# Kernel tuning notes

Hardware: AMD Instinct MI355X
Metric: run time of the kernel (lower is better)

## Reference

```python
import jax, jax.numpy as jnp
import numpy as np

DIM = 96        # N_VOX/2^(n_scales-layer) = 384/4 at finest layer
C = 24          # ch_in[2]
N_CUR = 150_000
N_GLB = 300_000
N_TGT = 100_000
N_GTGT = 200_000


def setup_inputs() -> dict:
    key = jax.random.key(0)
    ks = jax.random.split(key, 10)
    current_coords = jax.random.randint(ks[0], (N_CUR, 3), 0, DIM, dtype=jnp.int32)
    current_values = jax.random.normal(ks[1], (N_CUR, C), dtype=jnp.float32)
    # global coords live in the global frame; after subtracting the origin some fall outside [0, DIM)
    global_coords = jax.random.randint(ks[2], (N_GLB, 3), 0, DIM + 14, dtype=jnp.int32)
    global_value = jax.random.normal(ks[3], (N_GLB, C), dtype=jnp.float32)
    coords_target_global = jax.random.randint(ks[4], (N_TGT, 3), 0, DIM, dtype=jnp.int32)
    tsdf_target = jax.random.uniform(ks[5], (N_TGT,), minval=-1.0, maxval=1.0, dtype=jnp.float32)
    global_coords_target = jax.random.randint(ks[6], (N_GTGT, 3), 0, DIM + 14, dtype=jnp.int32)
    global_tsdf_target = jax.random.uniform(ks[7], (N_GTGT, 1), minval=-1.0, maxval=1.0, dtype=jnp.float32)
    relative_origin = jnp.array([5, 5, 5], dtype=jnp.int32)
    grid_mask = jax.random.randint(ks[8], (N_CUR,), 0, 2) > 0
    occupancy = jax.random.randint(ks[9], (N_CUR,), 0, 2) > 0
    return dict(current_coords=current_coords, current_values=current_values,
                global_coords=global_coords, global_value=global_value,
                coords_target_global=coords_target_global, tsdf_target=tsdf_target,
                global_coords_target=global_coords_target, global_tsdf_target=global_tsdf_target,
                relative_origin=relative_origin, grid_mask=grid_mask, occupancy=occupancy)


def _masked_idx(coords, mask, dim):
    # rows with mask==False get an out-of-range index -> dropped by scatter mode='drop'
    return jnp.where(mask[:, None], coords, dim)


def reference(current_coords, current_values, global_coords, global_value,
              coords_target_global, tsdf_target, global_coords_target,
              global_tsdf_target, relative_origin, grid_mask, occupancy):
    dim = DIM
    dtype = current_values.dtype
    c = current_values.shape[-1]

    # ---- shift global coords into local fragment frame; in-bounds test ----
    gc = global_coords - relative_origin                       # (Ng, 3)
    in_bounds = jnp.logical_and(gc >= 0, gc < dim).all(-1)     # (Ng,)

    # ---- valid_volume: True where a current voxel inside the camera frusta exists ----
    vi = _masked_idx(current_coords, grid_mask, dim)
    valid_volume = jnp.zeros((dim, dim, dim), dtype=bool).at[vi[:, 0], vi[:, 1], vi[:, 2]].set(True, mode='drop')

    # gather visibility at (clamped) global coords; out-of-bounds rows masked off
    gcc = jnp.clip(gc, 0, dim - 1)
    valid = in_bounds & valid_volume[gcc[:, 0], gcc[:, 1], gcc[:, 2]]   # == local_visible

    # ---- sparse -> dense feature volumes (feat_init = 0) ----
    gi = _masked_idx(gc, valid, dim)
    global_volume = jnp.zeros((dim, dim, dim, c), dtype=dtype).at[gi[:, 0], gi[:, 1], gi[:, 2]].set(global_value, mode='drop')
    cc = current_coords
    current_volume = jnp.zeros((dim, dim, dim, c), dtype=dtype).at[cc[:, 0], cc[:, 1], cc[:, 2]].set(current_values, mode='drop')

    # ---- occupancy volume & updated coordinate mask (dense mask == nonzero set) ----
    oi = _masked_idx(current_coords, occupancy, dim)
    occ_volume = jnp.zeros((dim, dim, dim), dtype=bool).at[oi[:, 0], oi[:, 1], oi[:, 2]].set(True, mode='drop')
    updated_mask = (global_volume != 0).any(-1) | occ_volume

    # voxels in FBV but not visible in current fragment (near set)
    near_mask = in_bounds & jnp.logical_not(valid)

    # ---- ground-truth TSDF fusion (default value = 1) ----
    gct = global_coords_target - relative_origin
    valid_target = jnp.logical_and(gct >= 0, gct < dim).all(-1)
    ti = _masked_idx(gct, valid_target, dim)
    target_volume = jnp.full((dim, dim, dim, 1), 1.0, dtype=dtype)
    target_volume = target_volume.at[ti[:, 0], ti[:, 1], ti[:, 2]].set(global_tsdf_target, mode='drop')
    ct = coords_target_global
    target_volume = target_volume.at[ct[:, 0], ct[:, 1], ct[:, 2]].set(tsdf_target[:, None], mode='drop')

    return (updated_mask, current_volume, global_volume, target_volume, valid, valid_target, near_mask)
```

## Files before the change

kernel.cpp:

```cpp
#include <hip/hip_runtime.h>

#define DIMV 96
#define CCH 24
#define NVOX (DIMV * DIMV * DIMV)
#define HALFV (NVOX / 2)
#define WORDS (NVOX / 32)
#define ZERO_INTS (2 * WORDS)
#define TOTAL_INTS (ZERO_INTS + 3 * NVOX)
#define N4I (TOTAL_INTS / 4)
#define NZERO4 (ZERO_INTS / 4)

#define PAYLOAD_BLOCKS (HALFV * 6 / 256)
#define MT_BLOCKS (NVOX / 1024)
#define RESOLVE_BLOCKS (PAYLOAD_BLOCKS + MT_BLOCKS)

typedef float v4f __attribute__((ext_vector_type(4)));
typedef int   v4i __attribute__((ext_vector_type(4)));
typedef int   v2i __attribute__((ext_vector_type(2)));

__global__ void init_detect_kernel(v4i* __restrict__ ws_vec,
                                   const unsigned int* __restrict__ mask_words,
                                   int* __restrict__ mode_p) {
    int i = blockIdx.x * blockDim.x + threadIdx.x;
    if (i < N4I) {
        int fill = (i < NZERO4) ? 0 : -1;
        v4i val = {fill, fill, fill, fill};
        ws_vec[i] = val;
    }
    if (blockIdx.x == 0) {
        __shared__ int s_byte, s_int, s_float;
        if (threadIdx.x == 0) { s_byte = 0; s_int = 0; s_float = 0; }
        __syncthreads();
        int flag = 0;
        for (int k = 0; k < 4; ++k) {
            unsigned int w = mask_words[threadIdx.x * 4 + k];
            if (w != 0u) {
                if (w == 1u)               flag |= 1;
                else if (w == 0x3F800000u) flag |= 2;
                else                       flag |= 4;
            }
        }
        if (flag & 1) atomicOr(&s_int, 1);
        if (flag & 2) atomicOr(&s_float, 1);
        if (flag & 4) atomicOr(&s_byte, 1);
        __syncthreads();
        if (threadIdx.x == 0)
            *mode_p = s_byte ? 0 : (s_float ? 2 : 1);
    }
}

__device__ __forceinline__ bool read_mask(const void* p, int i, int mode) {
    if (mode == 0) return ((const unsigned char*)p)[i] != 0;
    if (mode == 1) return ((const int*)p)[i] != 0;
    return ((const float*)p)[i] != 0.0f;
}

__global__ void scatter_cur_tgt_kernel(const int* __restrict__ coords,
                                       const void* __restrict__ grid_mask,
                                       const void* __restrict__ occupancy,
                                       const int* __restrict__ mode_p,
                                       unsigned int* __restrict__ valid_bits,
                                       unsigned int* __restrict__ occ_bits,
                                       int* __restrict__ key2,
                                       const int* __restrict__ gt_coords,
                                       const int* __restrict__ ct_coords,
                                       const int* __restrict__ origin,
                                       int* __restrict__ tgt_key,
                                       float* __restrict__ out_valid_target,
                                       int n_cur, int n_gtgt, int n_tgt) {
    int i = blockIdx.x * blockDim.x + threadIdx.x;
    if (i < n_cur) {
        int mode = *mode_p;
        int x = coords[3 * i], y = coords[3 * i + 1], z = coords[3 * i + 2];
        if ((unsigned)x >= DIMV || (unsigned)y >= DIMV || (unsigned)z >= DIMV) return;
        int v = (x * DIMV + y) * DIMV + z;
        if (read_mask(grid_mask, i, mode)) atomicOr(&valid_bits[v >> 5], 1u << (v & 31));
        if (read_mask(occupancy, i, mode)) atomicOr(&occ_bits[v >> 5], 1u << (v & 31));
        atomicMax(&key2[2 * v], i);
        return;
    }
    int j = i - n_cur;
    if (j < n_gtgt) {
        int x = gt_coords[3 * j] - origin[0];
        int y = gt_coords[3 * j + 1] - origin[1];
        int z = gt_coords[3 * j + 2] - origin[2];
        bool inb = (unsigned)x < DIMV && (unsigned)y < DIMV && (unsigned)z < DIMV;
        __builtin_nontemporal_store(inb ? 1.0f : 0.0f, &out_valid_target[j]);
        if (inb) atomicMax(&tgt_key[(x * DIMV + y) * DIMV + z], j);
        return;
    }
    int k = j - n_gtgt;
    if (k < n_tgt) {
        int x = ct_coords[3 * k], y = ct_coords[3 * k + 1], z = ct_coords[3 * k + 2];
        if ((unsigned)x < DIMV && (unsigned)y < DIMV && (unsigned)z < DIMV)
            atomicMax(&tgt_key[(x * DIMV + y) * DIMV + z], n_gtgt + k);
    }
}

__global__ void scatter_global_kernel(const int* __restrict__ gcoords,
                                      const int* __restrict__ origin,
                                      const unsigned int* __restrict__ valid_bits,
                                      int* __restrict__ key2,
                                      float* __restrict__ out_valid,
                                      float* __restrict__ out_near,
                                      int n) {
    int i = blockIdx.x * blockDim.x + threadIdx.x;
    if (i >= n) return;
    int x = gcoords[3 * i]     - origin[0];
    int y = gcoords[3 * i + 1] - origin[1];
    int z = gcoords[3 * i + 2] - origin[2];
    bool inb = (unsigned)x < DIMV && (unsigned)y < DIMV && (unsigned)z < DIMV;
    bool valid = false;
    if (inb) {
        int v = (x * DIMV + y) * DIMV + z;
        valid = (valid_bits[v >> 5] >> (v & 31)) & 1u;
        if (valid) atomicMax(&key2[2 * v + 1], i);
    }
    __builtin_nontemporal_store(valid ? 1.0f : 0.0f, &out_valid[i]);
    __builtin_nontemporal_store((inb && !valid) ? 1.0f : 0.0f, &out_near[i]);
}

__global__ void resolve_kernel(const v4f* __restrict__ cur_vals4,
                               const v4f* __restrict__ glb_vals4,
                               const float* __restrict__ tsdf_tgt,
                               const float* __restrict__ g_tsdf_tgt,
                               const v2i* __restrict__ key2_2,
                               const v4i* __restrict__ key2_4,
                               const v4i* __restrict__ tgt_key4,
                               const unsigned int* __restrict__ occ_bits,
                               v4f* __restrict__ out_mask4,
                               v4f* __restrict__ out_cur4,
                               v4f* __restrict__ out_glb4,
                               v4f* __restrict__ out_tgt4,
                               int n_gtgt) {
    int b = blockIdx.x;
    if (b < PAYLOAD_BLOCKS) {
        int idx = b * 256 + threadIdx.x;
        int p  = idx / 6;
        int c4 = idx - p * 6;
        int v0 = p, v1 = p + HALFV;

        v2i k0 = key2_2[v0];
        v2i k1 = key2_2[v1];

        v4f z = {0.f, 0.f, 0.f, 0.f};
        v4f a0 = (k0.x >= 0) ? __builtin_nontemporal_load(&cur_vals4[k0.x * 6 + c4]) : z;
        v4f a1 = (k1.x >= 0) ? __builtin_nontemporal_load(&cur_vals4[k1.x * 6 + c4]) : z;
        v4f b0 = (k0.y >= 0) ? __builtin_nontemporal_load(&glb_vals4[k0.y * 6 + c4]) : z;
        v4f b1 = (k1.y >= 0) ? __builtin_nontemporal_load(&glb_vals4[k1.y * 6 + c4]) : z;

        __builtin_nontemporal_store(a0, &out_cur4[idx]);
        __builtin_nontemporal_store(a1, &out_cur4[idx + HALFV * 6]);
        __builtin_nontemporal_store(b0, &out_glb4[idx]);
        __builtin_nontemporal_store(b1, &out_glb4[idx + HALFV * 6]);
        return;
    }
    {
        int t = (b - PAYLOAD_BLOCKS) * 256 + threadIdx.x;
        int v = 4 * t;
        v4i A = key2_4[2 * t];
        v4i B = key2_4[2 * t + 1];
        v4i T = tgt_key4[t];
        unsigned int occw = occ_bits[v >> 5] >> (v & 31);
        v4f m;
        m.x = (A.y >= 0 || (occw & 1u)) ? 1.0f : 0.0f;
        m.y = (A.w >= 0 || ((occw >> 1) & 1u)) ? 1.0f : 0.0f;
        m.z = (B.y >= 0 || ((occw >> 2) & 1u)) ? 1.0f : 0.0f;
        m.w = (B.w >= 0 || ((occw >> 3) & 1u)) ? 1.0f : 0.0f;
        v4f r;
        r.x = (T.x < 0) ? 1.0f : (T.x >= n_gtgt ? tsdf_tgt[T.x - n_gtgt] : g_tsdf_tgt[T.x]);
        r.y = (T.y < 0) ? 1.0f : (T.y >= n_gtgt ? tsdf_tgt[T.y - n_gtgt] : g_tsdf_tgt[T.y]);
        r.z = (T.z < 0) ? 1.0f : (T.z >= n_gtgt ? tsdf_tgt[T.z - n_gtgt] : g_tsdf_tgt[T.z]);
        r.w = (T.w < 0) ? 1.0f : (T.w >= n_gtgt ? tsdf_tgt[T.w - n_gtgt] : g_tsdf_tgt[T.w]);
        __builtin_nontemporal_store(m, &out_mask4[t]);
        __builtin_nontemporal_store(r, &out_tgt4[t]);
    }
}

extern "C" void kernel_launch(void* const* d_in, const int* in_sizes, int n_in,
                              void* d_out, int out_size, void* d_ws, size_t ws_size,
                              hipStream_t stream) {
    const int*   current_coords  = (const int*)  d_in[0];
    const float* current_values  = (const float*)d_in[1];
    const int*   global_coords   = (const int*)  d_in[2];
    const float* global_value    = (const float*)d_in[3];
    const int*   coords_target   = (const int*)  d_in[4];
    const float* tsdf_target     = (const float*)d_in[5];
    const int*   g_coords_target = (const int*)  d_in[6];
    const float* g_tsdf_target   = (const float*)d_in[7];
    const int*   origin          = (const int*)  d_in[8];
    const void*  grid_mask       = d_in[9];
    const void*  occupancy       = d_in[10];

    const int n_cur  = in_sizes[0] / 3;
    const int n_glb  = in_sizes[2] / 3;
    const int n_tgt  = in_sizes[4] / 3;
    const int n_gtgt = in_sizes[6] / 3;

    unsigned int* valid_bits = (unsigned int*)d_ws;
    unsigned int* occ_bits   = valid_bits + WORDS;
    int*          key2       = (int*)(occ_bits + WORDS);
    int*          tgt_key    = key2 + 2 * NVOX;
    int*          mode_p     = tgt_key + NVOX;

    float* out     = (float*)d_out;
    float* o_mask  = out;
    float* o_cur   = o_mask + NVOX;
    float* o_glb   = o_cur + NVOX * CCH;
    float* o_tgt   = o_glb + NVOX * CCH;
    float* o_valid = o_tgt + NVOX;
    float* o_vtgt  = o_valid + n_glb;
    float* o_near  = o_vtgt + n_gtgt;

    init_detect_kernel<<<(N4I + 255) / 256, 256, 0, stream>>>(
        (v4i*)d_ws, (const unsigned int*)grid_mask, mode_p);

    scatter_cur_tgt_kernel<<<(n_cur + n_gtgt + n_tgt + 255) / 256, 256, 0, stream>>>(
        current_coords, grid_mask, occupancy, mode_p, valid_bits, occ_bits, key2,
        g_coords_target, coords_target, origin, tgt_key, o_vtgt,
        n_cur, n_gtgt, n_tgt);

    scatter_global_kernel<<<(n_glb + 255) / 256, 256, 0, stream>>>(
        global_coords, origin, valid_bits, key2, o_valid, o_near, n_glb);

    resolve_kernel<<<RESOLVE_BLOCKS, 256, 0, stream>>>(
        (const v4f*)current_values, (const v4f*)global_value,
        tsdf_target, g_tsdf_target,
        (const v2i*)key2, (const v4i*)key2, (const v4i*)tgt_key, occ_bits,
        (v4f*)o_mask, (v4f*)o_cur, (v4f*)o_glb, (v4f*)o_tgt, n_gtgt);
}
```

Measured before the change: 267.2 us.

## Fuse four phases into one cooperative persistent kernel with grid syncs

Merges the init, the two scatter passes and the resolve pass into a single cooperative kernel with a fixed grid of 1024 blocks. Grid-stride loops replace the per-kernel grids, and grid.sync() stands in for the kernel boundaries. This is meant to remove three kernel launch gaps and the drain/fill between them. In exchange it adds grid-wide barrier cost and limits parallelism to the persistent grid. Launch bounds of 256x8 are assumed to let all blocks be co-resident.

```diff
diff --git a/kernel.cpp b/kernel.cpp
--- a/kernel.cpp
+++ b/kernel.cpp
@@ -1,4 +1,7 @@
 #include <hip/hip_runtime.h>
+#include <hip/hip_cooperative_groups.h>
+
+namespace cg = cooperative_groups;
 
 #define DIMV 96
 #define CCH 24
@@ -10,30 +13,61 @@
 #define N4I (TOTAL_INTS / 4)
 #define NZERO4 (ZERO_INTS / 4)
 
-#define PAYLOAD_BLOCKS (HALFV * 6 / 256)
-#define MT_BLOCKS (NVOX / 1024)
-#define RESOLVE_BLOCKS (PAYLOAD_BLOCKS + MT_BLOCKS)
+#define PAY (HALFV * 6)
+#define MT (NVOX / 4)
+#define GRID_BLOCKS 1024
 
 typedef float v4f __attribute__((ext_vector_type(4)));
 typedef int   v4i __attribute__((ext_vector_type(4)));
 typedef int   v2i __attribute__((ext_vector_type(2)));
 
-__global__ void init_detect_kernel(v4i* __restrict__ ws_vec,
-                                   const unsigned int* __restrict__ mask_words,
-                                   int* __restrict__ mode_p) {
-    int i = blockIdx.x * blockDim.x + threadIdx.x;
-    if (i < N4I) {
+struct Params {
+    const int*   coords;
+    const v4f*   cur_vals4;
+    const int*   gcoords;
+    const v4f*   glb_vals4;
+    const int*   ct_coords;
+    const float* tsdf_tgt;
+    const int*   gt_coords;
+    const float* g_tsdf_tgt;
+    const int*   origin;
+    const void*  grid_mask;
+    const void*  occupancy;
+    v4i*          ws_vec;
+    unsigned int* valid_bits;
+    unsigned int* occ_bits;
+    int*          key2;
+    int*          tgt_key;
+    int*          mode_p;
+    float* o_mask; v4f* o_cur4; v4f* o_glb4; float* o_tgt;
+    float* o_valid; float* o_vtgt; float* o_near;
+    int n_cur, n_glb, n_tgt, n_gtgt;
+};
+
+__device__ __forceinline__ bool read_mask(const void* p, int i, int mode) {
+    if (mode == 0) return ((const unsigned char*)p)[i] != 0;
+    if (mode == 1) return ((const int*)p)[i] != 0;
+    return ((const float*)p)[i] != 0.0f;
+}
+
+__global__ void __launch_bounds__(256, 8) fused_kernel(Params P) {
+    cg::grid_group grid = cg::this_grid();
+    const int NT  = GRID_BLOCKS * 256;
+    const int tid = blockIdx.x * blockDim.x + threadIdx.x;
+
+    for (int i = tid; i < N4I; i += NT) {
         int fill = (i < NZERO4) ? 0 : -1;
         v4i val = {fill, fill, fill, fill};
-        ws_vec[i] = val;
-    }
+        P.ws_vec[i] = val;
+    }
+    __shared__ int s_byte, s_int, s_float;
     if (blockIdx.x == 0) {
-        __shared__ int s_byte, s_int, s_float;
         if (threadIdx.x == 0) { s_byte = 0; s_int = 0; s_float = 0; }
         __syncthreads();
         int flag = 0;
+        const unsigned int* mw = (const unsigned int*)P.grid_mask;
         for (int k = 0; k < 4; ++k) {
-            unsigned int w = mask_words[threadIdx.x * 4 + k];
+            unsigned int w = mw[threadIdx.x * 4 + k];
             if (w != 0u) {
                 if (w == 1u)               flag |= 1;
                 else if (w == 0x3F800000u) flag |= 2;
@@ -45,153 +79,97 @@
         if (flag & 4) atomicOr(&s_byte, 1);
         __syncthreads();
         if (threadIdx.x == 0)
-            *mode_p = s_byte ? 0 : (s_float ? 2 : 1);
-    }
-}
-
-__device__ __forceinline__ bool read_mask(const void* p, int i, int mode) {
-    if (mode == 0) return ((const unsigned char*)p)[i] != 0;
-    if (mode == 1) return ((const int*)p)[i] != 0;
-    return ((const float*)p)[i] != 0.0f;
-}
-
-__global__ void scatter_cur_tgt_kernel(const int* __restrict__ coords,
-                                       const void* __restrict__ grid_mask,
-                                       const void* __restrict__ occupancy,
-                                       const int* __restrict__ mode_p,
-                                       unsigned int* __restrict__ valid_bits,
-                                       unsigned int* __restrict__ occ_bits,
-                                       int* __restrict__ key2,
-                                       const int* __restrict__ gt_coords,
-                                       const int* __restrict__ ct_coords,
-                                       const int* __restrict__ origin,
-                                       int* __restrict__ tgt_key,
-                                       float* __restrict__ out_valid_target,
-                                       int n_cur, int n_gtgt, int n_tgt) {
-    int i = blockIdx.x * blockDim.x + threadIdx.x;
-    if (i < n_cur) {
-        int mode = *mode_p;
-        int x = coords[3 * i], y = coords[3 * i + 1], z = coords[3 * i + 2];
-        if ((unsigned)x >= DIMV || (unsigned)y >= DIMV || (unsigned)z >= DIMV) return;
-        int v = (x * DIMV + y) * DIMV + z;
-        if (read_mask(grid_mask, i, mode)) atomicOr(&valid_bits[v >> 5], 1u << (v & 31));
-        if (read_mask(occupancy, i, mode)) atomicOr(&occ_bits[v >> 5], 1u << (v & 31));
-        atomicMax(&key2[2 * v], i);
-        return;
-    }
-    int j = i - n_cur;
-    if (j < n_gtgt) {
-        int x = gt_coords[3 * j] - origin[0];
-        int y = gt_coords[3 * j + 1] - origin[1];
-        int z = gt_coords[3 * j + 2] - origin[2];
+            *P.mode_p = s_byte ? 0 : (s_float ? 2 : 1);
+    }
+    grid.sync();
+
+    const int mode = *P.mode_p;
+    const int ox = P.origin[0], oy = P.origin[1], oz = P.origin[2];
+    const int n1 = P.n_cur + P.n_gtgt + P.n_tgt;
+    for (int i = tid; i < n1; i += NT) {
+        if (i < P.n_cur) {
+            int x = P.coords[3 * i], y = P.coords[3 * i + 1], z = P.coords[3 * i + 2];
+            if ((unsigned)x >= DIMV || (unsigned)y >= DIMV || (unsigned)z >= DIMV) continue;
+            int v = (x * DIMV + y) * DIMV + z;
+            if (read_mask(P.grid_mask, i, mode)) atomicOr(&P.valid_bits[v >> 5], 1u << (v & 31));
+            if (read_mask(P.occupancy, i, mode)) atomicOr(&P.occ_bits[v >> 5], 1u << (v & 31));
+            atomicMax(&P.key2[2 * v], i);
+        } else if (i < P.n_cur + P.n_gtgt) {
+            int j = i - P.n_cur;
+            int x = P.gt_coords[3 * j] - ox, y = P.gt_coords[3 * j + 1] - oy, z = P.gt_coords[3 * j + 2] - oz;
+            bool inb = (unsigned)x < DIMV && (unsigned)y < DIMV && (unsigned)z < DIMV;
+            __builtin_nontemporal_store(inb ? 1.0f : 0.0f, &P.o_vtgt[j]);
+            if (inb) atomicMax(&P.tgt_key[(x * DIMV + y) * DIMV + z], j);
+        } else {
+            int k = i - P.n_cur - P.n_gtgt;
+            int x = P.ct_coords[3 * k], y = P.ct_coords[3 * k + 1], z = P.ct_coords[3 * k + 2];
+            if ((unsigned)x < DIMV && (unsigned)y < DIMV && (unsigned)z < DIMV)
+                atomicMax(&P.tgt_key[(x * DIMV + y) * DIMV + z], P.n_gtgt + k);
+        }
+    }
+    grid.sync();
+
+    for (int i = tid; i < P.n_glb; i += NT) {
+        int x = P.gcoords[3 * i] - ox, y = P.gcoords[3 * i + 1] - oy, z = P.gcoords[3 * i + 2] - oz;
         bool inb = (unsigned)x < DIMV && (unsigned)y < DIMV && (unsigned)z < DIMV;
-        __builtin_nontemporal_store(inb ? 1.0f : 0.0f, &out_valid_target[j]);
-        if (inb) atomicMax(&tgt_key[(x * DIMV + y) * DIMV + z], j);
-        return;
-    }
-    int k = j - n_gtgt;
-    if (k < n_tgt) {
-        int x = ct_coords[3 * k], y = ct_coords[3 * k + 1], z = ct_coords[3 * k + 2];
-        if ((unsigned)x < DIMV && (unsigned)y < DIMV && (unsigned)z < DIMV)
-            atomicMax(&tgt_key[(x * DIMV + y) * DIMV + z], n_gtgt + k);
-    }
-}
-
-__global__ void scatter_global_kernel(const int* __restrict__ gcoords,
-                                      const int* __restrict__ origin,
-                                      const unsigned int* __restrict__ valid_bits,
-                                      int* __restrict__ key2,
-                                      float* __restrict__ out_valid,
-                                      float* __restrict__ out_near,
-                                      int n) {
-    int i = blockIdx.x * blockDim.x + threadIdx.x;
-    if (i >= n) return;
-    int x = gcoords[3 * i]     - origin[0];
-    int y = gcoords[3 * i + 1] - origin[1];
-    int z = gcoords[3 * i + 2] - origin[2];
-    bool inb = (unsigned)x < DIMV && (unsigned)y < DIMV && (unsigned)z < DIMV;
-    bool valid = false;
-    if (inb) {
-        int v = (x * DIMV + y) * DIMV + z;
-        valid = (valid_bits[v >> 5] >> (v & 31)) & 1u;
-        if (valid) atomicMax(&key2[2 * v + 1], i);
-    }
-    __builtin_nontemporal_store(valid ? 1.0f : 0.0f, &out_valid[i]);
-    __builtin_nontemporal_store((inb && !valid) ? 1.0f : 0.0f, &out_near[i]);
-}
-
-__global__ void resolve_kernel(const v4f* __restrict__ cur_vals4,
-                               const v4f* __restrict__ glb_vals4,
-                               const float* __restrict__ tsdf_tgt,
-                               const float* __restrict__ g_tsdf_tgt,
-                               const v2i* __restrict__ key2_2,
-                               const v4i* __restrict__ key2_4,
-                               const v4i* __restrict__ tgt_key4,
-                               const unsigned int* __restrict__ occ_bits,
-                               v4f* __restrict__ out_mask4,
-                               v4f* __restrict__ out_cur4,
-                               v4f* __restrict__ out_glb4,
-                               v4f* __restrict__ out_tgt4,
-                               int n_gtgt) {
-    int b = blockIdx.x;
-    if (b < PAYLOAD_BLOCKS) {
-        int idx = b * 256 + threadIdx.x;
-        int p  = idx / 6;
-        int c4 = idx - p * 6;
-        int v0 = p, v1 = p + HALFV;
-
-        v2i k0 = key2_2[v0];
-        v2i k1 = key2_2[v1];
-
-        v4f z = {0.f, 0.f, 0.f, 0.f};
-        v4f a0 = (k0.x >= 0) ? __builtin_nontemporal_load(&cur_vals4[k0.x * 6 + c4]) : z;
-        v4f a1 = (k1.x >= 0) ? __builtin_nontemporal_load(&cur_vals4[k1.x * 6 + c4]) : z;
-        v4f b0 = (k0.y >= 0) ? __builtin_nontemporal_load(&glb_vals4[k0.y * 6 + c4]) : z;
-        v4f b1 = (k1.y >= 0) ? __builtin_nontemporal_load(&glb_vals4[k1.y * 6 + c4]) : z;
-
-        __builtin_nontemporal_store(a0, &out_cur4[idx]);
-        __builtin_nontemporal_store(a1, &out_cur4[idx + HALFV * 6]);
-        __builtin_nontemporal_store(b0, &out_glb4[idx]);
-        __builtin_nontemporal_store(b1, &out_glb4[idx + HALFV * 6]);
-        return;
-    }
-    {
-        int t = (b - PAYLOAD_BLOCKS) * 256 + threadIdx.x;
-        int v = 4 * t;
-        v4i A = key2_4[2 * t];
-        v4i B = key2_4[2 * t + 1];
-        v4i T = tgt_key4[t];
-        unsigned int occw = occ_bits[v >> 5] >> (v & 31);
-        v4f m;
-        m.x = (A.y >= 0 || (occw & 1u)) ? 1.0f : 0.0f;
-        m.y = (A.w >= 0 || ((occw >> 1) & 1u)) ? 1.0f : 0.0f;
-        m.z = (B.y >= 0 || ((occw >> 2) & 1u)) ? 1.0f : 0.0f;
-        m.w = (B.w >= 0 || ((occw >> 3) & 1u)) ? 1.0f : 0.0f;
-        v4f r;
-        r.x = (T.x < 0) ? 1.0f : (T.x >= n_gtgt ? tsdf_tgt[T.x - n_gtgt] : g_tsdf_tgt[T.x]);
-        r.y = (T.y < 0) ? 1.0f : (T.y >= n_gtgt ? tsdf_tgt[T.y - n_gtgt] : g_tsdf_tgt[T.y]);
-        r.z = (T.z < 0) ? 1.0f : (T.z >= n_gtgt ? tsdf_tgt[T.z - n_gtgt] : g_tsdf_tgt[T.z]);
-        r.w = (T.w < 0) ? 1.0f : (T.w >= n_gtgt ? tsdf_tgt[T.w - n_gtgt] : g_tsdf_tgt[T.w]);
-        __builtin_nontemporal_store(m, &out_mask4[t]);
-        __builtin_nontemporal_store(r, &out_tgt4[t]);
+        bool valid = false;
+        if (inb) {
+            int v = (x * DIMV + y) * DIMV + z;
+            valid = (P.valid_bits[v >> 5] >> (v & 31)) & 1u;
+            if (valid) atomicMax(&P.key2[2 * v + 1], i);
+        }
+        __builtin_nontemporal_store(valid ? 1.0f : 0.0f, &P.o_valid[i]);
+        __builtin_nontemporal_store((inb && !valid) ? 1.0f : 0.0f, &P.o_near[i]);
+    }
+    grid.sync();
+
+    const v2i* key2_2 = (const v2i*)P.key2;
+    const v4i* key2_4 = (const v4i*)P.key2;
+    const v4i* tgt4   = (const v4i*)P.tgt_key;
+    v4f* out_mask4 = (v4f*)P.o_mask;
+    v4f* out_tgt4  = (v4f*)P.o_tgt;
+    const int total3 = PAY + MT;
+    for (int i = tid; i < total3; i += NT) {
+        if (i < PAY) {
+            int p  = i / 6;
+            int c4 = i - p * 6;
+            v2i k0 = key2_2[p];
+            v2i k1 = key2_2[p + HALFV];
+            v4f z = {0.f, 0.f, 0.f, 0.f};
+            v4f a0 = (k0.x >= 0) ? __builtin_nontemporal_load(&P.cur_vals4[k0.x * 6 + c4]) : z;
+            v4f a1 = (k1.x >= 0) ? __builtin_nontemporal_load(&P.cur_vals4[k1.x * 6 + c4]) : z;
+            v4f b0 = (k0.y >= 0) ? __builtin_nontemporal_load(&P.glb_vals4[k0.y * 6 + c4]) : z;
+            v4f b1 = (k1.y >= 0) ? __builtin_nontemporal_load(&P.glb_vals4[k1.y * 6 + c4]) : z;
+            __builtin_nontemporal_store(a0, &P.o_cur4[i]);
+            __builtin_nontemporal_store(a1, &P.o_cur4[i + PAY]);
+            __builtin_nontemporal_store(b0, &P.o_glb4[i]);
+            __builtin_nontemporal_store(b1, &P.o_glb4[i + PAY]);
+        } else {
+            int t = i - PAY;
+            int v = 4 * t;
+            v4i A = key2_4[2 * t];
+            v4i B = key2_4[2 * t + 1];
+            v4i T = tgt4[t];
+            unsigned int occw = P.occ_bits[v >> 5] >> (v & 31);
+            v4f m;
+            m.x = (A.y >= 0 || (occw & 1u)) ? 1.0f : 0.0f;
+            m.y = (A.w >= 0 || ((occw >> 1) & 1u)) ? 1.0f : 0.0f;
+            m.z = (B.y >= 0 || ((occw >> 2) & 1u)) ? 1.0f : 0.0f;
+            m.w = (B.w >= 0 || ((occw >> 3) & 1u)) ? 1.0f : 0.0f;
+            v4f r;
+            r.x = (T.x < 0) ? 1.0f : (T.x >= P.n_gtgt ? P.tsdf_tgt[T.x - P.n_gtgt] : P.g_tsdf_tgt[T.x]);
+            r.y = (T.y < 0) ? 1.0f : (T.y >= P.n_gtgt ? P.tsdf_tgt[T.y - P.n_gtgt] : P.g_tsdf_tgt[T.y]);
+            r.z = (T.z < 0) ? 1.0f : (T.z >= P.n_gtgt ? P.tsdf_tgt[T.z - P.n_gtgt] : P.g_tsdf_tgt[T.z]);
+            r.w = (T.w < 0) ? 1.0f : (T.w >= P.n_gtgt ? P.tsdf_tgt[T.w - P.n_gtgt] : P.g_tsdf_tgt[T.w]);
+            __builtin_nontemporal_store(m, &out_mask4[t]);
+            __builtin_nontemporal_store(r, &out_tgt4[t]);
+        }
     }
 }
 
 extern "C" void kernel_launch(void* const* d_in, const int* in_sizes, int n_in,
                               void* d_out, int out_size, void* d_ws, size_t ws_size,
                               hipStream_t stream) {
-    const int*   current_coords  = (const int*)  d_in[0];
-    const float* current_values  = (const float*)d_in[1];
-    const int*   global_coords   = (const int*)  d_in[2];
-    const float* global_value    = (const float*)d_in[3];
-    const int*   coords_target   = (const int*)  d_in[4];
-    const float* tsdf_target     = (const float*)d_in[5];
-    const int*   g_coords_target = (const int*)  d_in[6];
-    const float* g_tsdf_target   = (const float*)d_in[7];
-    const int*   origin          = (const int*)  d_in[8];
-    const void*  grid_mask       = d_in[9];
-    const void*  occupancy       = d_in[10];
-
     const int n_cur  = in_sizes[0] / 3;
     const int n_glb  = in_sizes[2] / 3;
     const int n_tgt  = in_sizes[4] / 3;
@@ -212,20 +190,29 @@
     float* o_vtgt  = o_valid + n_glb;
     float* o_near  = o_vtgt + n_gtgt;
 
-    init_detect_kernel<<<(N4I + 255) / 256, 256, 0, stream>>>(
-        (v4i*)d_ws, (const unsigned int*)grid_mask, mode_p);
-
-    scatter_cur_tgt_kernel<<<(n_cur + n_gtgt + n_tgt + 255) / 256, 256, 0, stream>>>(
-        current_coords, grid_mask, occupancy, mode_p, valid_bits, occ_bits, key2,
-        g_coords_target, coords_target, origin, tgt_key, o_vtgt,
-        n_cur, n_gtgt, n_tgt);
-
-    scatter_global_kernel<<<(n_glb + 255) / 256, 256, 0, stream>>>(
-        global_coords, origin, valid_bits, key2, o_valid, o_near, n_glb);
-
-    resolve_kernel<<<RESOLVE_BLOCKS, 256, 0, stream>>>(
-        (const v4f*)current_values, (const v4f*)global_value,
-        tsdf_target, g_tsdf_target,
-        (const v2i*)key2, (const v4i*)key2, (const v4i*)tgt_key, occ_bits,
-        (v4f*)o_mask, (v4f*)o_cur, (v4f*)o_glb, (v4f*)o_tgt, n_gtgt);
+    Params P;
+    P.coords     = (const int*)  d_in[0];
+    P.cur_vals4  = (const v4f*)  d_in[1];
+    P.gcoords    = (const int*)  d_in[2];
+    P.glb_vals4  = (const v4f*)  d_in[3];
+    P.ct_coords  = (const int*)  d_in[4];
+    P.tsdf_tgt   = (const float*)d_in[5];
+    P.gt_coords  = (const int*)  d_in[6];
+    P.g_tsdf_tgt = (const float*)d_in[7];
+    P.origin     = (const int*)  d_in[8];
+    P.grid_mask  = d_in[9];
+    P.occupancy  = d_in[10];
+    P.ws_vec     = (v4i*)d_ws;
+    P.valid_bits = valid_bits;
+    P.occ_bits   = occ_bits;
+    P.key2       = key2;
+    P.tgt_key    = tgt_key;
+    P.mode_p     = mode_p;
+    P.o_mask = o_mask;  P.o_cur4 = (v4f*)o_cur;  P.o_glb4 = (v4f*)o_glb;
+    P.o_tgt  = o_tgt;   P.o_valid = o_valid;     P.o_vtgt = o_vtgt;  P.o_near = o_near;
+    P.n_cur = n_cur; P.n_glb = n_glb; P.n_tgt = n_tgt; P.n_gtgt = n_gtgt;
+
+    void* kargs[] = { &P };
+    hipLaunchCooperativeKernel((void*)fused_kernel, dim3(GRID_BLOCKS), dim3(256),
+                               kargs, 0, stream);
 }
```

Result: slower. 628.0 us (+135.0%).
